# Performance work log

Hardware: AMD Instinct MI355X
Metric: run time of the kernel (lower is better)

The kernel has to match this reference:

```python
import jax, jax.numpy as jnp
import numpy as np

N_NODES = 50000
N_EDGES = 600000
D = 128


def setup_inputs() -> dict:
    key = jax.random.key(0)
    k1, k2, k3 = jax.random.split(key, 3)
    x = jax.random.normal(k1, (N_NODES, D), dtype=jnp.float32)
    # Glorot-like init for the GCN linear weight
    W = jax.random.normal(k2, (D, D), dtype=jnp.float32) * (1.0 / np.sqrt(D))
    b = jnp.zeros((D,), dtype=jnp.float32)
    edge_index = jax.random.randint(k3, (2, N_EDGES), 0, N_NODES, dtype=jnp.int64)
    edge_attr = jnp.zeros((N_EDGES,), dtype=jnp.float32)   # unused by this layer
    batch = jnp.zeros((N_NODES,), dtype=jnp.int64)          # unused by this layer
    y = jnp.zeros((N_NODES,), dtype=jnp.int64)              # unused by this layer
    return {"x": x, "W": W, "b": b, "edge_index": edge_index,
            "edge_attr": edge_attr, "batch": batch, "y": y}


def reference(x, W, b, edge_index, edge_attr, batch, y):
    # GCNConv with default add_self_loops=True, symmetric normalization,
    # followed by ReLU (dropout disabled since GNNdrop == 0).
    N = x.shape[0]
    self_loops = jnp.arange(N, dtype=edge_index.dtype)
    src = jnp.concatenate([edge_index[0], self_loops])  # [E+N]
    dst = jnp.concatenate([edge_index[1], self_loops])  # [E+N]

    # Degree over destination nodes (includes self-loops)
    ones = jnp.ones(src.shape[0], dtype=x.dtype)
    deg = jax.ops.segment_sum(ones, dst, num_segments=N)          # [N]
    dinv = jnp.where(deg > 0, jax.lax.rsqrt(deg), 0.0)            # deg^{-1/2}
    norm = dinv[src] * dinv[dst]                                   # [E+N]

    # Linear transform first (as PyG GCNConv does), then gather-scale-scatter
    h = x @ W                                                      # [N, D]
    msg = h[src] * norm[:, None]                                   # [E+N, D]
    out = jax.ops.segment_sum(msg, dst, num_segments=N) + b       # [N, D]
    return jax.nn.relu(out)
```

## Files before the change

kernel.cpp:

```cpp
#include <hip/hip_runtime.h>

#define D 128
#define NBH 256
#define CAP 4096

typedef __attribute__((ext_vector_type(8))) short bf16x8;
typedef __attribute__((ext_vector_type(4))) float f32x4;
typedef __attribute__((ext_vector_type(8))) unsigned short us8;
typedef __attribute__((ext_vector_type(4))) int i32x4;

static __device__ __forceinline__ float bf2f(unsigned short u) {
    union { unsigned int i; float f; } c; c.i = ((unsigned int)u) << 16; return c.f;
}
static __device__ __forceinline__ unsigned short f2bf(float f) {
    union { float f; unsigned int i; } c; c.f = f;
    unsigned int r = c.i + 0x7FFFu + ((c.i >> 16) & 1u);
    return (unsigned short)(r >> 16);
}

__global__ __launch_bounds__(256) void k_wprep(const float* __restrict__ W,
                                               unsigned short* __restrict__ Wt) {
    int t = (int)blockIdx.x * 256 + (int)threadIdx.x;
    int k = t >> 7, c = t & 127;
    Wt[c * D + k] = f2bf(W[t]);
}

__global__ __launch_bounds__(256) void k_gemm_hist(const float* __restrict__ x,
                                                   const unsigned short* __restrict__ Wt,
                                                   const int* __restrict__ dst,
                                                   int* __restrict__ counts2d,
                                                   unsigned short* __restrict__ hs,
                                                   int N, int E, int nbuck) {
    if ((int)blockIdx.x < NBH) {
        __shared__ int bins[1024];
        for (int t = threadIdx.x; t < nbuck; t += 256) bins[t] = 0;
        __syncthreads();
        const int k = (int)blockIdx.x;
        const long long stride = (long long)NBH * 1024;
        for (long long i = ((long long)k * 256 + threadIdx.x) * 4; i < E; i += stride) {
            if (i + 4 <= E) {
                i32x4 d = *(const i32x4*)(dst + i);
                atomicAdd(&bins[d.x >> 6], 1);
                atomicAdd(&bins[d.y >> 6], 1);
                atomicAdd(&bins[d.z >> 6], 1);
                atomicAdd(&bins[d.w >> 6], 1);
            } else {
                for (long long j = i; j < E; ++j) atomicAdd(&bins[dst[j] >> 6], 1);
            }
        }
        __syncthreads();
        for (int t = threadIdx.x; t < nbuck; t += 256)
            counts2d[t * NBH + k] = bins[t];
        return;
    }

    const int wave = threadIdx.x >> 6;
    const int l    = threadIdx.x & 63;
    const int m0   = ((int)blockIdx.x - NBH) * 64 + wave * 16;
    const int lr   = l & 15;
    const int kg   = l >> 4;
    const int row_a = m0 + lr;

    f32x4 acc[8];
#pragma unroll
    for (int t = 0; t < 8; ++t) acc[t] = (f32x4){0.f, 0.f, 0.f, 0.f};

#pragma unroll
    for (int kk = 0; kk < 4; ++kk) {
        const int kbase = kk * 32 + kg * 8;
        bf16x8 afrag;
        if (row_a < N) {
            const float* xp = x + (size_t)row_a * D + kbase;
            f32x4 x0 = *(const f32x4*)xp;
            f32x4 x1 = *(const f32x4*)(xp + 4);
#pragma unroll
            for (int j = 0; j < 4; ++j) afrag[j] = (short)f2bf(x0[j]);
#pragma unroll
            for (int j = 0; j < 4; ++j) afrag[4 + j] = (short)f2bf(x1[j]);
        } else {
#pragma unroll
            for (int j = 0; j < 8; ++j) afrag[j] = 0;
        }
#pragma unroll
        for (int nt = 0; nt < 8; ++nt) {
            bf16x8 bfrag = *(const bf16x8*)(Wt + (size_t)(nt * 16 + lr) * D + kbase);
            acc[nt] = __builtin_amdgcn_mfma_f32_16x16x32_bf16(afrag, bfrag, acc[nt], 0, 0, 0);
        }
    }

#pragma unroll
    for (int j = 0; j < 4; ++j) {
        int row = m0 + kg * 4 + j;
        if (row < N) {
#pragma unroll
            for (int nt = 0; nt < 8; ++nt)
                hs[(size_t)row * D + nt * 16 + lr] = f2bf(acc[nt][j]);
        }
    }
}

__global__ __launch_bounds__(256) void k_colscan(int* __restrict__ counts2d,
                                                 int* __restrict__ btot) {
    __shared__ int ts[256];
    const int b = (int)blockIdx.x;
    const int t = (int)threadIdx.x;
    int c = counts2d[b * NBH + t];
    ts[t] = c;
    __syncthreads();
    for (int off = 1; off < 256; off <<= 1) {
        int v = (t >= off) ? ts[t - off] : 0;
        __syncthreads();
        ts[t] += v;
        __syncthreads();
    }
    counts2d[b * NBH + t] = ts[t] - c;
    if (t == 255) btot[b] = ts[255];
}

__global__ __launch_bounds__(1024) void k_btscan(const int* __restrict__ btot,
                                                 int* __restrict__ offsets, int nbuck) {
    __shared__ int ts[1024];
    const int b = (int)threadIdx.x;
    int v = (b < nbuck) ? btot[b] : 0;
    ts[b] = v;
    __syncthreads();
    for (int off = 1; off < 1024; off <<= 1) {
        int t = (b >= off) ? ts[b - off] : 0;
        __syncthreads();
        ts[b] += t;
        __syncthreads();
    }
    if (b < nbuck) offsets[b + 1] = ts[b];
    if (b == 0) offsets[0] = 0;
}

__global__ __launch_bounds__(256) void k_scatter(const int* __restrict__ src,
                                                 const int* __restrict__ dst,
                                                 const int* __restrict__ offsets,
                                                 const int* __restrict__ counts2d,
                                                 unsigned int* __restrict__ sorted,
                                                 int E, int nbuck) {
    __shared__ int base_l[1024];
    __shared__ int cur[1024];
    const int k = (int)blockIdx.x;
    for (int t = threadIdx.x; t < nbuck; t += 256) {
        base_l[t] = offsets[t] + counts2d[t * NBH + k];
        cur[t] = 0;
    }
    __syncthreads();

    const long long stride = (long long)NBH * 1024;
    for (long long i = ((long long)k * 256 + threadIdx.x) * 4; i < E; i += stride) {
        if (i + 4 <= E) {
            i32x4 d = *(const i32x4*)(dst + i);
            i32x4 s = *(const i32x4*)(src + i);
            int p;
            p = base_l[d.x >> 6] + atomicAdd(&cur[d.x >> 6], 1);
            sorted[p] = (unsigned int)(s.x & 0xFFFF) | ((unsigned int)(d.x & 63) << 16);
            p = base_l[d.y >> 6] + atomicAdd(&cur[d.y >> 6], 1);
            sorted[p] = (unsigned int)(s.y & 0xFFFF) | ((unsigned int)(d.y & 63) << 16);
            p = base_l[d.z >> 6] + atomicAdd(&cur[d.z >> 6], 1);
            sorted[p] = (unsigned int)(s.z & 0xFFFF) | ((unsigned int)(d.z & 63) << 16);
            p = base_l[d.w >> 6] + atomicAdd(&cur[d.w >> 6], 1);
            sorted[p] = (unsigned int)(s.w & 0xFFFF) | ((unsigned int)(d.w & 63) << 16);
        } else {
            for (long long j = i; j < E; ++j) {
                int dd = dst[j], ss = src[j];
                int p = base_l[dd >> 6] + atomicAdd(&cur[dd >> 6], 1);
                sorted[p] = (unsigned int)(ss & 0xFFFF) | ((unsigned int)(dd & 63) << 16);
            }
        }
    }
}

__global__ __launch_bounds__(256) void k_dinv(const unsigned int* __restrict__ sorted,
                                              const int* __restrict__ offsets,
                                              float* __restrict__ dinv, int N) {
    __shared__ int bins[64];
    const int b = (int)blockIdx.x;
    if (threadIdx.x < 64) bins[threadIdx.x] = 0;
    __syncthreads();
    const int off = offsets[b];
    const int cnt = offsets[b + 1] - off;
    for (int i = threadIdx.x; i < cnt; i += 256)
        atomicAdd(&bins[(sorted[off + i] >> 16) & 63], 1);
    __syncthreads();
    if (threadIdx.x < 64) {
        int v = b * 64 + (int)threadIdx.x;
        if (v < N) dinv[v] = rsqrtf((float)(bins[threadIdx.x] + 1));
    }
}

__global__ __launch_bounds__(512) void k_aggregate(const unsigned short* __restrict__ hs,
                                                   const unsigned int* __restrict__ sorted,
                                                   const int* __restrict__ offsets,
                                                   const float* __restrict__ dinv,
                                                   const float* __restrict__ bias,
                                                   float* __restrict__ out, int N) {
    __shared__ unsigned short srt[CAP];
    __shared__ int bins[64];
    __shared__ int boff[64];
    __shared__ int cur[64];

    const int bb  = (int)blockIdx.x;
    const int off = offsets[bb];
    const int cnt = offsets[bb + 1] - off;
    const bool fits = (cnt <= CAP);

    if (fits) {
        if (threadIdx.x < 64) bins[threadIdx.x] = 0;
        __syncthreads();
        for (int i = threadIdx.x; i < cnt; i += 512)
            atomicAdd(&bins[(sorted[off + i] >> 16) & 63], 1);
        __syncthreads();
        if (threadIdx.x < 64) {
            const int lane = (int)threadIdx.x;
            int bv = bins[lane];
            int inc = bv;
            for (int o = 1; o < 64; o <<= 1) {
                int t = __shfl_up(inc, o, 64);
                if (lane >= o) inc += t;
            }
            boff[lane] = inc - bv;
            cur[lane] = 0;
        }
        __syncthreads();
        for (int i = threadIdx.x; i < cnt; i += 512) {
            unsigned int e = sorted[off + i];
            int dl = (int)((e >> 16) & 63u);
            int p = boff[dl] + atomicAdd(&cur[dl], 1);
            srt[p] = (unsigned short)(e & 0xFFFFu);
        }
        __syncthreads();
    }

    const int grp  = (int)(threadIdx.x >> 4);
    const int lane = (int)(threadIdx.x & 15);
    const f32x4 b0 = *(const f32x4*)(bias + lane * 8);
    const f32x4 b1 = *(const f32x4*)(bias + lane * 8 + 4);

    for (int pass = 0; pass < 2; ++pass) {
        const int vl = pass * 32 + grp;
        const int v  = bb * 64 + vl;
        if (v >= N) continue;

        const float dv = dinv[v];
        float acc[8];
        {
            us8 h = *(const us8*)(hs + (size_t)v * D + lane * 8);
#pragma unroll
            for (int j = 0; j < 8; ++j) acc[j] = bf2f(h[j]) * dv;
        }

        if (fits) {
            int i   = boff[vl];
            int end = i + bins[vl];
            for (; i + 4 <= end; i += 4) {
                int s0 = srt[i + 0];
                int s1 = srt[i + 1];
                int s2 = srt[i + 2];
                int s3 = srt[i + 3];
                float d0 = dinv[s0], d1 = dinv[s1], d2 = dinv[s2], d3 = dinv[s3];
                us8 m0 = *(const us8*)(hs + (size_t)s0 * D + lane * 8);
                us8 m1 = *(const us8*)(hs + (size_t)s1 * D + lane * 8);
                us8 m2 = *(const us8*)(hs + (size_t)s2 * D + lane * 8);
                us8 m3 = *(const us8*)(hs + (size_t)s3 * D + lane * 8);
#pragma unroll
                for (int j = 0; j < 8; ++j)
                    acc[j] += (bf2f(m0[j]) * d0 + bf2f(m1[j]) * d1)
                            + (bf2f(m2[j]) * d2 + bf2f(m3[j]) * d3);
            }
            for (; i < end; ++i) {
                int s = srt[i];
                float ds = dinv[s];
                us8 m = *(const us8*)(hs + (size_t)s * D + lane * 8);
#pragma unroll
                for (int j = 0; j < 8; ++j) acc[j] += bf2f(m[j]) * ds;
            }
        } else {
            for (int i = 0; i < cnt; ++i) {
                unsigned int e = sorted[off + i];
                if ((int)((e >> 16) & 63u) == vl) {
                    int s = (int)(e & 0xFFFFu);
                    float ds = dinv[s];
                    us8 m = *(const us8*)(hs + (size_t)s * D + lane * 8);
#pragma unroll
                    for (int j = 0; j < 8; ++j) acc[j] += bf2f(m[j]) * ds;
                }
            }
        }

        f32x4 o0, o1;
#pragma unroll
        for (int j = 0; j < 4; ++j) {
            o0[j] = fmaxf(fmaf(acc[j],     dv, b0[j]), 0.0f);
            o1[j] = fmaxf(fmaf(acc[4 + j], dv, b1[j]), 0.0f);
        }
        float* op = out + (size_t)v * D + lane * 8;
        *(f32x4*)op       = o0;
        *(f32x4*)(op + 4) = o1;
    }
}

static inline char* align_up(char* p, size_t a) {
    return (char*)(((uintptr_t)p + a - 1) & ~(uintptr_t)(a - 1));
}

extern "C" void kernel_launch(void* const* d_in, const int* in_sizes, int n_in,
                              void* d_out, int out_size, void* d_ws, size_t ws_size,
                              hipStream_t stream) {
    const float* x  = (const float*)d_in[0];
    const float* W  = (const float*)d_in[1];
    const float* b  = (const float*)d_in[2];
    const int*   ei = (const int*)d_in[3];

    const int N = in_sizes[0] / D;
    const int E = in_sizes[3] / 2;
    const int* src = ei;
    const int* dst = ei + E;

    const int nbuck = (N + 63) >> 6;

    char* p = (char*)d_ws;
    int* counts2d        = (int*)p;            p = align_up(p + sizeof(int) * nbuck * NBH, 64);
    int* btot            = (int*)p;            p = align_up(p + sizeof(int) * nbuck, 64);
    int* offsets         = (int*)p;            p = align_up(p + sizeof(int) * (nbuck + 1), 64);
    unsigned int* sorted = (unsigned int*)p;   p = align_up(p + sizeof(unsigned int) * E, 64);
    float* dinv          = (float*)p;          p = align_up(p + sizeof(float) * N, 64);
    unsigned short* Wt   = (unsigned short*)p; p = align_up(p + sizeof(short) * D * D, 64);
    unsigned short* hs   = (unsigned short*)p;

    float* out = (float*)d_out;

    const int gemm_blks = (N + 63) / 64;

    k_wprep<<<(D * D) / 256, 256, 0, stream>>>(W, Wt);
    k_gemm_hist<<<NBH + gemm_blks, 256, 0, stream>>>(x, Wt, dst, counts2d, hs, N, E, nbuck);
    k_colscan<<<nbuck, 256, 0, stream>>>(counts2d, btot);
    k_btscan<<<1, 1024, 0, stream>>>(btot, offsets, nbuck);
    k_scatter<<<NBH, 256, 0, stream>>>(src, dst, offsets, counts2d, sorted, E, nbuck);
    k_dinv<<<nbuck, 256, 0, stream>>>(sorted, offsets, dinv, N);
    k_aggregate<<<nbuck, 512, 0, stream>>>(hs, sorted, offsets, dinv, b, out, N);
}
```

Measured before the change: 84.95 us.

## Regroup launches to merge wprep with histogram and colscan with GEMM; interleave aggregation

Weight conversion now runs as extra blocks inside the histogram kernel, and the column scan runs as extra blocks inside the GEMM kernel. This removes one kernel launch and lets independent work share a grid. Separately, the aggregate kernel processes both of its destination nodes at the same time, interleaving their neighbor gathers to expose more memory-level parallelism. The cost is more registers per thread and some tail-loop code duplication.

```diff
diff --git a/kernel.cpp b/kernel.cpp
--- a/kernel.cpp
+++ b/kernel.cpp
@@ -18,45 +18,65 @@
     return (unsigned short)(r >> 16);
 }
 
-__global__ __launch_bounds__(256) void k_wprep(const float* __restrict__ W,
-                                               unsigned short* __restrict__ Wt) {
-    int t = (int)blockIdx.x * 256 + (int)threadIdx.x;
-    int k = t >> 7, c = t & 127;
-    Wt[c * D + k] = f2bf(W[t]);
-}
-
-__global__ __launch_bounds__(256) void k_gemm_hist(const float* __restrict__ x,
-                                                   const unsigned short* __restrict__ Wt,
-                                                   const int* __restrict__ dst,
-                                                   int* __restrict__ counts2d,
-                                                   unsigned short* __restrict__ hs,
-                                                   int N, int E, int nbuck) {
-    if ((int)blockIdx.x < NBH) {
-        __shared__ int bins[1024];
-        for (int t = threadIdx.x; t < nbuck; t += 256) bins[t] = 0;
-        __syncthreads();
-        const int k = (int)blockIdx.x;
-        const long long stride = (long long)NBH * 1024;
-        for (long long i = ((long long)k * 256 + threadIdx.x) * 4; i < E; i += stride) {
-            if (i + 4 <= E) {
-                i32x4 d = *(const i32x4*)(dst + i);
-                atomicAdd(&bins[d.x >> 6], 1);
-                atomicAdd(&bins[d.y >> 6], 1);
-                atomicAdd(&bins[d.z >> 6], 1);
-                atomicAdd(&bins[d.w >> 6], 1);
-            } else {
-                for (long long j = i; j < E; ++j) atomicAdd(&bins[dst[j] >> 6], 1);
-            }
-        }
-        __syncthreads();
-        for (int t = threadIdx.x; t < nbuck; t += 256)
-            counts2d[t * NBH + k] = bins[t];
+__global__ __launch_bounds__(256) void k_hist_wprep(const int* __restrict__ dst,
+                                                    int* __restrict__ counts2d,
+                                                    const float* __restrict__ W,
+                                                    unsigned short* __restrict__ Wt,
+                                                    int E, int nbuck) {
+    if ((int)blockIdx.x >= NBH) {
+        int t = ((int)blockIdx.x - NBH) * 256 + (int)threadIdx.x;
+        int k = t >> 7, c = t & 127;
+        Wt[c * D + k] = f2bf(W[t]);
+        return;
+    }
+    __shared__ int bins[1024];
+    for (int t = threadIdx.x; t < nbuck; t += 256) bins[t] = 0;
+    __syncthreads();
+    const int k = (int)blockIdx.x;
+    const long long stride = (long long)NBH * 1024;
+    for (long long i = ((long long)k * 256 + threadIdx.x) * 4; i < E; i += stride) {
+        if (i + 4 <= E) {
+            i32x4 d = *(const i32x4*)(dst + i);
+            atomicAdd(&bins[d.x >> 6], 1);
+            atomicAdd(&bins[d.y >> 6], 1);
+            atomicAdd(&bins[d.z >> 6], 1);
+            atomicAdd(&bins[d.w >> 6], 1);
+        } else {
+            for (long long j = i; j < E; ++j) atomicAdd(&bins[dst[j] >> 6], 1);
+        }
+    }
+    __syncthreads();
+    for (int t = threadIdx.x; t < nbuck; t += 256)
+        counts2d[t * NBH + k] = bins[t];
+}
+
+__global__ __launch_bounds__(256) void k_gemm_colscan(const float* __restrict__ x,
+                                                      const unsigned short* __restrict__ Wt,
+                                                      int* __restrict__ counts2d,
+                                                      int* __restrict__ btot,
+                                                      unsigned short* __restrict__ hs,
+                                                      int N, int nbuck) {
+    if ((int)blockIdx.x < nbuck) {
+        __shared__ int ts[256];
+        const int b = (int)blockIdx.x;
+        const int t = (int)threadIdx.x;
+        int c = counts2d[b * NBH + t];
+        ts[t] = c;
+        __syncthreads();
+        for (int off = 1; off < 256; off <<= 1) {
+            int v = (t >= off) ? ts[t - off] : 0;
+            __syncthreads();
+            ts[t] += v;
+            __syncthreads();
+        }
+        counts2d[b * NBH + t] = ts[t] - c;
+        if (t == 255) btot[b] = ts[255];
         return;
     }
 
     const int wave = threadIdx.x >> 6;
     const int l    = threadIdx.x & 63;
-    const int m0   = ((int)blockIdx.x - NBH) * 64 + wave * 16;
+    const int m0   = ((int)blockIdx.x - nbuck) * 64 + wave * 16;
     const int lr   = l & 15;
     const int kg   = l >> 4;
     const int row_a = m0 + lr;
@@ -97,24 +117,6 @@
                 hs[(size_t)row * D + nt * 16 + lr] = f2bf(acc[nt][j]);
         }
     }
-}
-
-__global__ __launch_bounds__(256) void k_colscan(int* __restrict__ counts2d,
-                                                 int* __restrict__ btot) {
-    __shared__ int ts[256];
-    const int b = (int)blockIdx.x;
-    const int t = (int)threadIdx.x;
-    int c = counts2d[b * NBH + t];
-    ts[t] = c;
-    __syncthreads();
-    for (int off = 1; off < 256; off <<= 1) {
-        int v = (t >= off) ? ts[t - off] : 0;
-        __syncthreads();
-        ts[t] += v;
-        __syncthreads();
-    }
-    counts2d[b * NBH + t] = ts[t] - c;
-    if (t == 255) btot[b] = ts[255];
 }
 
 __global__ __launch_bounds__(1024) void k_btscan(const int* __restrict__ btot,
@@ -239,64 +241,128 @@
     const f32x4 b0 = *(const f32x4*)(bias + lane * 8);
     const f32x4 b1 = *(const f32x4*)(bias + lane * 8 + 4);
 
-    for (int pass = 0; pass < 2; ++pass) {
-        const int vl = pass * 32 + grp;
-        const int v  = bb * 64 + vl;
-        if (v >= N) continue;
-
-        const float dv = dinv[v];
-        float acc[8];
-        {
-            us8 h = *(const us8*)(hs + (size_t)v * D + lane * 8);
-#pragma unroll
-            for (int j = 0; j < 8; ++j) acc[j] = bf2f(h[j]) * dv;
-        }
-
-        if (fits) {
-            int i   = boff[vl];
-            int end = i + bins[vl];
-            for (; i + 4 <= end; i += 4) {
-                int s0 = srt[i + 0];
-                int s1 = srt[i + 1];
-                int s2 = srt[i + 2];
-                int s3 = srt[i + 3];
-                float d0 = dinv[s0], d1 = dinv[s1], d2 = dinv[s2], d3 = dinv[s3];
-                us8 m0 = *(const us8*)(hs + (size_t)s0 * D + lane * 8);
-                us8 m1 = *(const us8*)(hs + (size_t)s1 * D + lane * 8);
-                us8 m2 = *(const us8*)(hs + (size_t)s2 * D + lane * 8);
-                us8 m3 = *(const us8*)(hs + (size_t)s3 * D + lane * 8);
-#pragma unroll
-                for (int j = 0; j < 8; ++j)
-                    acc[j] += (bf2f(m0[j]) * d0 + bf2f(m1[j]) * d1)
-                            + (bf2f(m2[j]) * d2 + bf2f(m3[j]) * d3);
+    const int vlA = grp;
+    const int vlB = 32 + grp;
+    const int vA  = bb * 64 + vlA;
+    const int vB  = bb * 64 + vlB;
+    const bool okA = (vA < N);
+    const bool okB = (vB < N);
+
+    float dvA = 0.f, dvB = 0.f;
+    float accA[8], accB[8];
+#pragma unroll
+    for (int j = 0; j < 8; ++j) { accA[j] = 0.f; accB[j] = 0.f; }
+
+    if (okA) {
+        dvA = dinv[vA];
+        us8 h = *(const us8*)(hs + (size_t)vA * D + lane * 8);
+#pragma unroll
+        for (int j = 0; j < 8; ++j) accA[j] = bf2f(h[j]) * dvA;
+    }
+    if (okB) {
+        dvB = dinv[vB];
+        us8 h = *(const us8*)(hs + (size_t)vB * D + lane * 8);
+#pragma unroll
+        for (int j = 0; j < 8; ++j) accB[j] = bf2f(h[j]) * dvB;
+    }
+
+    if (fits) {
+        int iA = 0, endA = 0, iB = 0, endB = 0;
+        if (okA) { iA = boff[vlA]; endA = iA + bins[vlA]; }
+        if (okB) { iB = boff[vlB]; endB = iB + bins[vlB]; }
+
+        while (iA + 2 <= endA && iB + 2 <= endB) {
+            int sa0 = srt[iA + 0], sa1 = srt[iA + 1]; iA += 2;
+            int sb0 = srt[iB + 0], sb1 = srt[iB + 1]; iB += 2;
+            float da0 = dinv[sa0], da1 = dinv[sa1];
+            float db0 = dinv[sb0], db1 = dinv[sb1];
+            us8 ma0 = *(const us8*)(hs + (size_t)sa0 * D + lane * 8);
+            us8 ma1 = *(const us8*)(hs + (size_t)sa1 * D + lane * 8);
+            us8 mb0 = *(const us8*)(hs + (size_t)sb0 * D + lane * 8);
+            us8 mb1 = *(const us8*)(hs + (size_t)sb1 * D + lane * 8);
+#pragma unroll
+            for (int j = 0; j < 8; ++j) {
+                accA[j] += bf2f(ma0[j]) * da0 + bf2f(ma1[j]) * da1;
+                accB[j] += bf2f(mb0[j]) * db0 + bf2f(mb1[j]) * db1;
             }
-            for (; i < end; ++i) {
-                int s = srt[i];
+        }
+        for (; iA + 4 <= endA; iA += 4) {
+            int s0 = srt[iA + 0], s1 = srt[iA + 1], s2 = srt[iA + 2], s3 = srt[iA + 3];
+            float d0 = dinv[s0], d1 = dinv[s1], d2 = dinv[s2], d3 = dinv[s3];
+            us8 m0 = *(const us8*)(hs + (size_t)s0 * D + lane * 8);
+            us8 m1 = *(const us8*)(hs + (size_t)s1 * D + lane * 8);
+            us8 m2 = *(const us8*)(hs + (size_t)s2 * D + lane * 8);
+            us8 m3 = *(const us8*)(hs + (size_t)s3 * D + lane * 8);
+#pragma unroll
+            for (int j = 0; j < 8; ++j)
+                accA[j] += (bf2f(m0[j]) * d0 + bf2f(m1[j]) * d1)
+                         + (bf2f(m2[j]) * d2 + bf2f(m3[j]) * d3);
+        }
+        for (; iA < endA; ++iA) {
+            int s = srt[iA];
+            float ds = dinv[s];
+            us8 m = *(const us8*)(hs + (size_t)s * D + lane * 8);
+#pragma unroll
+            for (int j = 0; j < 8; ++j) accA[j] += bf2f(m[j]) * ds;
+        }
+        for (; iB + 4 <= endB; iB += 4) {
+            int s0 = srt[iB + 0], s1 = srt[iB + 1], s2 = srt[iB + 2], s3 = srt[iB + 3];
+            float d0 = dinv[s0], d1 = dinv[s1], d2 = dinv[s2], d3 = dinv[s3];
+            us8 m0 = *(const us8*)(hs + (size_t)s0 * D + lane * 8);
+            us8 m1 = *(const us8*)(hs + (size_t)s1 * D + lane * 8);
+            us8 m2 = *(const us8*)(hs + (size_t)s2 * D + lane * 8);
+            us8 m3 = *(const us8*)(hs + (size_t)s3 * D + lane * 8);
+#pragma unroll
+            for (int j = 0; j < 8; ++j)
+                accB[j] += (bf2f(m0[j]) * d0 + bf2f(m1[j]) * d1)
+                         + (bf2f(m2[j]) * d2 + bf2f(m3[j]) * d3);
+        }
+        for (; iB < endB; ++iB) {
+            int s = srt[iB];
+            float ds = dinv[s];
+            us8 m = *(const us8*)(hs + (size_t)s * D + lane * 8);
+#pragma unroll
+            for (int j = 0; j < 8; ++j) accB[j] += bf2f(m[j]) * ds;
+        }
+    } else {
+        for (int i = 0; i < cnt; ++i) {
+            unsigned int e = sorted[off + i];
+            int dl = (int)((e >> 16) & 63u);
+            int s  = (int)(e & 0xFFFFu);
+            if (okA && dl == vlA) {
                 float ds = dinv[s];
                 us8 m = *(const us8*)(hs + (size_t)s * D + lane * 8);
 #pragma unroll
-                for (int j = 0; j < 8; ++j) acc[j] += bf2f(m[j]) * ds;
+                for (int j = 0; j < 8; ++j) accA[j] += bf2f(m[j]) * ds;
             }
-        } else {
-            for (int i = 0; i < cnt; ++i) {
-                unsigned int e = sorted[off + i];
-                if ((int)((e >> 16) & 63u) == vl) {
-                    int s = (int)(e & 0xFFFFu);
-                    float ds = dinv[s];
-                    us8 m = *(const us8*)(hs + (size_t)s * D + lane * 8);
-#pragma unroll
-                    for (int j = 0; j < 8; ++j) acc[j] += bf2f(m[j]) * ds;
-                }
+            if (okB && dl == vlB) {
+                float ds = dinv[s];
+                us8 m = *(const us8*)(hs + (size_t)s * D + lane * 8);
+#pragma unroll
+                for (int j = 0; j < 8; ++j) accB[j] += bf2f(m[j]) * ds;
             }
         }
-
+    }
+
+    if (okA) {
         f32x4 o0, o1;
 #pragma unroll
         for (int j = 0; j < 4; ++j) {
-            o0[j] = fmaxf(fmaf(acc[j],     dv, b0[j]), 0.0f);
-            o1[j] = fmaxf(fmaf(acc[4 + j], dv, b1[j]), 0.0f);
-        }
-        float* op = out + (size_t)v * D + lane * 8;
+            o0[j] = fmaxf(fmaf(accA[j],     dvA, b0[j]), 0.0f);
+            o1[j] = fmaxf(fmaf(accA[4 + j], dvA, b1[j]), 0.0f);
+        }
+        float* op = out + (size_t)vA * D + lane * 8;
+        *(f32x4*)op       = o0;
+        *(f32x4*)(op + 4) = o1;
+    }
+    if (okB) {
+        f32x4 o0, o1;
+#pragma unroll
+        for (int j = 0; j < 4; ++j) {
+            o0[j] = fmaxf(fmaf(accB[j],     dvB, b0[j]), 0.0f);
+            o1[j] = fmaxf(fmaf(accB[4 + j], dvB, b1[j]), 0.0f);
+        }
+        float* op = out + (size_t)vB * D + lane * 8;
         *(f32x4*)op       = o0;
         *(f32x4*)(op + 4) = o1;
     }
@@ -334,9 +400,8 @@
 
     const int gemm_blks = (N + 63) / 64;
 
-    k_wprep<<<(D * D) / 256, 256, 0, stream>>>(W, Wt);
-    k_gemm_hist<<<NBH + gemm_blks, 256, 0, stream>>>(x, Wt, dst, counts2d, hs, N, E, nbuck);
-    k_colscan<<<nbuck, 256, 0, stream>>>(counts2d, btot);
+    k_hist_wprep<<<NBH + (D * D) / 256, 256, 0, stream>>>(dst, counts2d, W, Wt, E, nbuck);
+    k_gemm_colscan<<<nbuck + gemm_blks, 256, 0, stream>>>(x, Wt, counts2d, btot, hs, N, nbuck);
     k_btscan<<<1, 1024, 0, stream>>>(btot, offsets, nbuck);
     k_scatter<<<NBH, 256, 0, stream>>>(src, dst, offsets, counts2d, sorted, E, nbuck);
     k_dinv<<<nbuck, 256, 0, stream>>>(sorted, offsets, dinv, N);
```

Result: slower. 88.71 us (+4.4%).
